# Kernel optimization log

Hardware: AMD Instinct MI355X
Metric: run time of the kernel (lower is better)

## Reference

```python
import jax, jax.numpy as jnp
import numpy as np

D_MODEL = 1024
N_HEADS = 16
D_HEAD = D_MODEL // N_HEADS


def setup_inputs() -> dict:
    key = jax.random.key(0)
    kx, kq, kk, kv = jax.random.split(key, 4)
    B, T = 2, 2048
    X = jax.random.normal(kx, (B, T, D_MODEL), dtype=jnp.float32)
    s = 1.0 / np.sqrt(D_MODEL)
    # torch nn.Linear weight is [out, in]; y = x @ W.T
    Wq = jax.random.uniform(kq, (D_MODEL, D_MODEL), jnp.float32, -s, s)
    Wk = jax.random.uniform(kk, (D_MODEL, D_MODEL), jnp.float32, -s, s)
    Wv = jax.random.uniform(kv, (D_MODEL, D_MODEL), jnp.float32, -s, s)
    return {"X": X, "Wq": Wq, "Wk": Wk, "Wv": Wv}


def reference(X, Wq, Wk, Wv):
    B, T, _ = X.shape
    def heads(W):
        # x @ W.T -> [B,T,D] -> [B,H,T,Dh]
        return (X @ W.T).reshape(B, T, N_HEADS, D_HEAD).transpose(0, 2, 1, 3)
    Q, K, V = heads(Wq), heads(Wk), heads(Wv)
    scores = jnp.einsum('bhqd,bhkd->bhqk', Q, K)
    causal = jnp.tril(jnp.ones((T, T), dtype=bool))
    # original masks with -inf BEFORE scaling; -inf/scale == -inf, so equivalent
    scores = jnp.where(causal, scores, -jnp.inf) / jnp.sqrt(jnp.float32(D_HEAD))
    attn = jax.nn.softmax(scores, axis=-1)
    out = jnp.einsum('bhqk,bhkd->bhqd', attn, V)
    return out.transpose(0, 2, 1, 3).reshape(B, T, N_HEADS * D_HEAD)
```

## Files before the change

### kernel.cpp

```cpp
#include <hip/hip_runtime.h>


using bf16x8   = __attribute__((ext_vector_type(8))) __bf16;
using floatx4  = __attribute__((ext_vector_type(4))) float;
using floatx16 = __attribute__((ext_vector_type(16))) float;
using uintx4   = __attribute__((ext_vector_type(4))) unsigned int;

#define T_SEQ   2048
#define D_MODEL 1024
#define N_HEADS 16
#define D_HEAD  64
#define BATCH   2
#define M_TOT   4096
#define N_TOT   3072
#define PLANE   (T_SEQ * D_HEAD)
#define NX      (M_TOT * D_MODEL)
#define NWSEG   (D_MODEL * D_MODEL)
#define QSCALE  0.18033688f
#define SM_BIAS 24.0f

__device__ __forceinline__ unsigned short f32_to_bf16(float f) {
  unsigned int u = __float_as_uint(f);
  u += 0x7fffu + ((u >> 16) & 1u);
  return (unsigned short)(u >> 16);
}
__device__ __forceinline__ unsigned int pack2_bf16(float a, float b) {
  unsigned int ua = __float_as_uint(a) + 0x8000u;
  unsigned int ub = __float_as_uint(b) + 0x8000u;
  return __builtin_amdgcn_perm(ub, ua, 0x07060302);
}
__device__ __forceinline__ void async_cp16(void* lds, const void* gptr) {
  __builtin_amdgcn_global_load_lds(
      (const __attribute__((address_space(1))) unsigned int*)gptr,
      (__attribute__((address_space(3))) unsigned int*)lds, 16, 0, 0);
}

__global__ __launch_bounds__(256) void cvt_kernel(
    const float* __restrict__ X,  const float* __restrict__ Wq,
    const float* __restrict__ Wk, const float* __restrict__ Wv,
    unsigned short* __restrict__ Xb, unsigned short* __restrict__ Wb)
{
  const size_t i = ((size_t)blockIdx.x * 256 + threadIdx.x) * 8;
  const float* src;
  unsigned short* dst;
  if (i < NX) { src = X + i; dst = Xb + i; }
  else {
    const size_t r = i - NX;
    const int w = (int)(r >> 20);
    const size_t o = r & (NWSEG - 1);
    src = ((w == 0) ? Wq : (w == 1) ? Wk : Wv) + o;
    dst = Wb + r;
  }
  float4 f0 = *(const float4*)src;
  float4 f1 = *(const float4*)(src + 4);
  uint4 out;
  out.x = pack2_bf16(f0.x, f0.y);
  out.y = pack2_bf16(f0.z, f0.w);
  out.z = pack2_bf16(f1.x, f1.y);
  out.w = pack2_bf16(f1.z, f1.w);
  *(uint4*)dst = out;
}

__global__ __launch_bounds__(256) void gemm_qkv(
    const unsigned short* __restrict__ Xb,
    const unsigned short* __restrict__ Wb,
    unsigned short* __restrict__ Qb,
    unsigned short* __restrict__ Kb,
    unsigned short* __restrict__ VTb)
{
  __shared__ unsigned short Als[128 * 64];
  __shared__ unsigned short Bls[128 * 64];

  const int tid  = threadIdx.x;
  const int lane = tid & 63;
  const int wave = tid >> 6;
  const int l15  = lane & 15;
  const int quad = lane >> 4;
  const int wm   = wave >> 1, wn = wave & 1;

  const int n_blk = blockIdx.x * 128;
  const int m_blk = blockIdx.y * 128;

  const int swz = (((tid >> 3) ^ tid) & 7) * 8;
  const unsigned short* Ag = Xb + (size_t)(m_blk + (tid >> 3)) * D_MODEL + swz;
  const unsigned short* Bg = Wb + (size_t)(n_blk + (tid >> 3)) * D_MODEL + swz;
  char* Alds = (char*)Als + wave * 1024;
  char* Blds = (char*)Bls + wave * 1024;

  floatx4 acc[4][4] = {};

  for (int k0 = 0; k0 < D_MODEL; k0 += 64) {
    __syncthreads();
#pragma unroll
    for (int p = 0; p < 4; p++) {
      async_cp16(Alds + p * 4096, Ag + (size_t)p * 32 * D_MODEL + k0);
      async_cp16(Blds + p * 4096, Bg + (size_t)p * 32 * D_MODEL + k0);
    }
    __syncthreads();

#pragma unroll
    for (int ks = 0; ks < 2; ks++) {
      bf16x8 a[4], b[4];
#pragma unroll
      for (int i = 0; i < 4; i++) {
        const int sa = ((ks * 4 + quad) ^ (l15 & 7)) * 16;
        a[i] = *(const bf16x8*)((char*)Als + (wm * 64 + 16 * i + l15) * 128 + sa);
        b[i] = *(const bf16x8*)((char*)Bls + (wn * 64 + 16 * i + l15) * 128 + sa);
      }
#pragma unroll
      for (int mi = 0; mi < 4; mi++)
#pragma unroll
        for (int ni = 0; ni < 4; ni++)
          acc[mi][ni] = __builtin_amdgcn_mfma_f32_16x16x32_bf16(a[mi], b[ni], acc[mi][ni], 0, 0, 0);
    }
  }

  __syncthreads();
  char* ep = (char*)Als + wave * 8192;
  const int w_sel  = n_blk >> 10;
  const int m_base = m_blk + wm * 64;
  const int n_base = n_blk + wn * 64;
  const int h      = (n_base & 1023) >> 6;
  const float csc  = (w_sel == 0) ? QSCALE : 1.0f;

  if (w_sel < 2) {
#pragma unroll
    for (int mi = 0; mi < 4; mi++)
#pragma unroll
      for (int ni = 0; ni < 4; ni++)
#pragma unroll
        for (int r = 0; r < 4; r++) {
          const int row  = 16 * mi + quad * 4 + r;
          const int colb = (16 * ni + l15) * 2;
          const int phys = ((colb >> 4) ^ (row & 7)) * 16;
          *(unsigned short*)(ep + row * 128 + phys + (colb & 15)) =
              f32_to_bf16(acc[mi][ni][r] * csc);
        }
  } else {
#pragma unroll
    for (int mi = 0; mi < 4; mi++)
#pragma unroll
      for (int ni = 0; ni < 4; ni++)
#pragma unroll
        for (int r = 0; r < 4; r++) {
          const int row  = 16 * ni + l15;
          const int colb = (16 * mi + quad * 4 + r) * 2;
          const int phys = ((colb >> 4) ^ (row & 7)) * 16;
          *(unsigned short*)(ep + row * 128 + phys + (colb & 15)) =
              f32_to_bf16(acc[mi][ni][r]);
        }
  }
  asm volatile("s_waitcnt lgkmcnt(0)" ::: "memory");

#pragma unroll
  for (int pass = 0; pass < 8; pass++) {
    const int row  = pass * 8 + (lane >> 3);
    const int phys = ((lane & 7) ^ (row & 7)) * 16;
    uint4 v = *(const uint4*)(ep + row * 128 + phys);
    if (w_sel < 2) {
      const int m  = m_base + row;
      const int bb = m >> 11;
      const int t  = m & (T_SEQ - 1);
      unsigned short* dst = ((w_sel == 0) ? Qb : Kb) +
          ((size_t)(bb * N_HEADS + h) * T_SEQ + t) * D_HEAD + (lane & 7) * 8;
      *(uint4*)dst = v;
    } else {
      const int bb = m_base >> 11;
      unsigned short* dst = VTb +
          ((size_t)(bb * N_HEADS + h) * D_HEAD + row) * T_SEQ + (m_base & (T_SEQ - 1)) + (lane & 7) * 8;
      *(uint4*)dst = v;
    }
  }
}

__global__ __launch_bounds__(256) void attn_kernel(
    const unsigned short* __restrict__ Qb,
    const unsigned short* __restrict__ Kb,
    const unsigned short* __restrict__ VTb,
    float* __restrict__ Out)
{
  __shared__ __align__(16) char smem[65536];

  const int tid  = threadIdx.x;
  const int lane = tid & 63;
  const int wave = tid >> 6;
  const int l31  = lane & 31;
  const int q1   = lane >> 5;
  const int wq   = wave & 1;
  const int wk   = wave >> 1;

  const int bh   = blockIdx.x & 31;
  const int pair = blockIdx.x >> 5;

  const unsigned short* Qp = Qb  + (size_t)bh * PLANE;
  const unsigned short* Kp = Kb  + (size_t)bh * PLANE;
  const unsigned short* Vp = VTb + (size_t)bh * PLANE;

  const int swz = (((tid >> 3) ^ tid) & 7) * 8;
  const unsigned short* Kg = Kp + (size_t)(tid >> 3) * D_HEAD + swz;
  const unsigned short* Vg = Vp + (size_t)(tid >> 3) * T_SEQ + swz;
  const int b = bh >> 4, h = bh & 15;

  float* const LB = (float*)(smem + 33792);

#define STAGE_CHUNK(c)                                                        \
  do {                                                                        \
    char* kd = smem + (((c) >> 1) & 1) * 16384 + ((c) & 1) * 8192;            \
    char* vd = smem + 32768 + (((c) >> 1) & 1) * 16384 + ((c) & 1) * 8192;    \
    _Pragma("unroll")                                                         \
    for (int p = 0; p < 2; p++) {                                             \
      async_cp16(kd + p * 4096 + wave * 1024,                                 \
                 Kg + (size_t)((c) * 64 + p * 32) * D_HEAD);                  \
      async_cp16(vd + p * 4096 + wave * 1024,                                 \
                 Vg + (size_t)(p * 32) * T_SEQ + (c) * 64);                   \
    }                                                                         \
  } while (0)

#pragma unroll 1
  for (int it = 0; it < 2; it++) {
    const int strip = it ? (31 - pair) : pair;
    const int qbase = strip * 64 + wq * 32;
    const int nch   = strip + 1;

    bf16x8 aq[4];
#pragma unroll
    for (int kp = 0; kp < 4; kp++)
      aq[kp] = *(const bf16x8*)(Qp + (size_t)(qbase + l31) * D_HEAD + kp * 16 + q1 * 8);

    floatx16 o0 = {}, o1 = {};
    float l_acc = 0.0f;

    __syncthreads();

    STAGE_CHUNK(0);
    if (nch > 1) STAGE_CHUNK(1);

#pragma unroll 1
    for (int j2 = 0; j2 < nch; j2 += 2) {
      __syncthreads();
      if (j2 + 2 < nch) STAGE_CHUNK(j2 + 2);
      if (j2 + 3 < nch) STAGE_CHUNK(j2 + 3);

#pragma unroll
      for (int u = 0; u < 2; u++) {
        const int jc = j2 + u;
        if (jc >= nch) break;
        const char* Ksb = smem + ((jc >> 1) & 1) * 16384 + (jc & 1) * 8192;
        const char* Vsb = smem + 32768 + ((jc >> 1) & 1) * 16384 + (jc & 1) * 8192;
        const int kbase = jc * 64 + wk * 32;

        if (kbase <= qbase + 31) {
          floatx16 s = {};
          const int krow = wk * 32 + l31;
          __builtin_amdgcn_s_setprio(1);
#pragma unroll
          for (int kp = 0; kp < 4; kp++) {
            const int phys = (((2 * kp + q1) ^ (krow & 7)) * 16);
            bf16x8 ak = *(const bf16x8*)(Ksb + krow * 128 + phys);
            s = __builtin_amdgcn_mfma_f32_32x32x16_bf16(ak, aq[kp], s, 0, 0, 0);
          }
          __builtin_amdgcn_s_setprio(0);

          if (kbase >= qbase) {
            const int q = qbase + l31;
#pragma unroll
            for (int r = 0; r < 16; r++) {
              const int kk = kbase + (r & 3) + 8 * (r >> 2) + 4 * q1;
              if (kk > q) s[r] = -INFINITY;
            }
          }

          float pv[16];
#pragma unroll
          for (int r = 0; r < 16; r++)
            pv[r] = __builtin_amdgcn_exp2f(s[r] - SM_BIAS);
#pragma unroll
          for (int r = 0; r < 16; r += 4)
            l_acc += (pv[r] + pv[r + 1]) + (pv[r + 2] + pv[r + 3]);

          unsigned int w[8];
#pragma unroll
          for (int m = 0; m < 8; m++)
            asm("v_cvt_pk_bf16_f32 %0, %1, %2" : "=v"(w[m]) : "v"(pv[2 * m]), "v"(pv[2 * m + 1]));

          __builtin_amdgcn_s_setprio(1);
#pragma unroll
          for (int kp = 0; kp < 2; kp++) {
            unsigned int b0 = w[4 * kp],     b2 = w[4 * kp + 2];
            unsigned int b1 = w[4 * kp + 1], b3 = w[4 * kp + 3];
            asm("v_permlane32_swap_b32 %0, %1" : "+v"(b0), "+v"(b2));
            asm("v_permlane32_swap_b32 %0, %1" : "+v"(b1), "+v"(b3));
            uintx4 uu; uu[0] = b0; uu[1] = b1; uu[2] = b2; uu[3] = b3;
            const bf16x8 pf = __builtin_bit_cast(bf16x8, uu);

            const int c = 4 * wk + 2 * kp + q1;
            const int row0 = l31;
            bf16x8 av0 = *(const bf16x8*)(Vsb + row0 * 128 + ((c ^ (row0 & 7)) * 16));
            o0 = __builtin_amdgcn_mfma_f32_32x32x16_bf16(av0, pf, o0, 0, 0, 0);
            const int row1 = 32 + l31;
            bf16x8 av1 = *(const bf16x8*)(Vsb + row1 * 128 + ((c ^ (row1 & 7)) * 16));
            o1 = __builtin_amdgcn_mfma_f32_32x32x16_bf16(av1, pf, o1, 0, 0, 0);
          }
          __builtin_amdgcn_s_setprio(0);
        }
      }
    }

    float la = l_acc, lb2 = l_acc;
    asm("v_permlane32_swap_b32 %0, %1" : "+v"(la), "+v"(lb2));
    const float lt = la + lb2;

    __syncthreads();

    float* ob = (float*)smem + (wk * 2 + wq) * (64 * 33);
#pragma unroll
    for (int r = 0; r < 16; r++) {
      const int d0 = (r & 3) + 8 * (r >> 2) + 4 * q1;
      ob[d0 * 33 + l31]        = o0[r];
      ob[(32 + d0) * 33 + l31] = o1[r];
    }
    if (lane < 32) LB[wk * 64 + wq * 32 + l31] = lt;
    __syncthreads();

    const int row = tid >> 2;
    const int dg  = tid & 3;
    const int wqr = row >> 5, ql = row & 31;
    const float inv = 1.0f / (LB[row] + LB[64 + row]);
    const float* obA = (const float*)smem + (0 * 2 + wqr) * (64 * 33);
    const float* obB = (const float*)smem + (1 * 2 + wqr) * (64 * 33);

    float vout[16];
#pragma unroll
    for (int i = 0; i < 16; i++) {
      const int d = dg * 16 + i;
      vout[i] = (obA[d * 33 + ql] + obB[d * 33 + ql]) * inv;
    }
    const int t = strip * 64 + row;
    float* dst = Out + (size_t)(b * T_SEQ + t) * D_MODEL + h * D_HEAD + dg * 16;
#pragma unroll
    for (int m = 0; m < 4; m++)
      *(float4*)(dst + 4 * m) = *(const float4*)(vout + 4 * m);
  }
#undef STAGE_CHUNK
}

extern "C" void kernel_launch(void* const* d_in, const int* in_sizes, int n_in,
                              void* d_out, int out_size, void* d_ws, size_t ws_size,
                              hipStream_t stream) {
  const float* X  = (const float*)d_in[0];
  const float* Wq = (const float*)d_in[1];
  const float* Wk = (const float*)d_in[2];
  const float* Wv = (const float*)d_in[3];

  unsigned short* Qb = (unsigned short*)d_ws;
  unsigned short* Kb = Qb + (size_t)BATCH * N_HEADS * T_SEQ * D_HEAD;
  unsigned short* VT = Kb + (size_t)BATCH * N_HEADS * T_SEQ * D_HEAD;

  unsigned short* Xb = (unsigned short*)d_out;
  unsigned short* Wb = Xb + (size_t)NX;

  cvt_kernel<<<3584, 256, 0, stream>>>(X, Wq, Wk, Wv, Xb, Wb);

  dim3 g1(N_TOT / 128, M_TOT / 128);
  gemm_qkv<<<g1, 256, 0, stream>>>(Xb, Wb, Qb, Kb, VT);

  attn_kernel<<<512, 256, 0, stream>>>(Qb, Kb, VT, (float*)d_out);
}
```

Baseline: 149.8 us.

## Split attention into 32-query strips with four waves splitting keys

The attention kernel now gives each block a 32-row query strip instead of 64 rows. All four waves share the same queries and each takes a different 32-key slice of a 128-key chunk, and the grid doubles to 1024 blocks. The multi-chunk async double-buffered K/V staging is replaced by a single 128-key buffer that is loaded and synchronized every iteration. This cuts LDS use and raises block count and occupancy, but it loses overlap between loads and compute, adds two barriers per chunk, and makes the final cross-wave reduction four-way.

```diff
diff --git a/kernel.cpp b/kernel.cpp
--- a/kernel.cpp
+++ b/kernel.cpp
@@ -179,15 +179,13 @@
     const unsigned short* __restrict__ VTb,
     float* __restrict__ Out)
 {
-  __shared__ __align__(16) char smem[65536];
+  __shared__ __align__(16) char smem[34304];
 
   const int tid  = threadIdx.x;
   const int lane = tid & 63;
   const int wave = tid >> 6;
   const int l31  = lane & 31;
   const int q1   = lane >> 5;
-  const int wq   = wave & 1;
-  const int wk   = wave >> 1;
 
   const int bh   = blockIdx.x & 31;
   const int pair = blockIdx.x >> 5;
@@ -195,32 +193,22 @@
   const unsigned short* Qp = Qb  + (size_t)bh * PLANE;
   const unsigned short* Kp = Kb  + (size_t)bh * PLANE;
   const unsigned short* Vp = VTb + (size_t)bh * PLANE;
-
-  const int swz = (((tid >> 3) ^ tid) & 7) * 8;
-  const unsigned short* Kg = Kp + (size_t)(tid >> 3) * D_HEAD + swz;
-  const unsigned short* Vg = Vp + (size_t)(tid >> 3) * T_SEQ + swz;
   const int b = bh >> 4, h = bh & 15;
 
+  const int sl4 = ((tid & 15) ^ (tid >> 4)) & 15;
+  const unsigned short* Kg0 =
+      Kp + (size_t)((tid >> 4) + 64 * (sl4 >> 3)) * D_HEAD + (sl4 & 7) * 8;
+  const unsigned short* Vg0 = Vp + (size_t)(tid >> 4) * T_SEQ + sl4 * 8;
+
+  char* const Ks = smem;
+  char* const Vs = smem + 16384;
   float* const LB = (float*)(smem + 33792);
-
-#define STAGE_CHUNK(c)                                                        \
-  do {                                                                        \
-    char* kd = smem + (((c) >> 1) & 1) * 16384 + ((c) & 1) * 8192;            \
-    char* vd = smem + 32768 + (((c) >> 1) & 1) * 16384 + ((c) & 1) * 8192;    \
-    _Pragma("unroll")                                                         \
-    for (int p = 0; p < 2; p++) {                                             \
-      async_cp16(kd + p * 4096 + wave * 1024,                                 \
-                 Kg + (size_t)((c) * 64 + p * 32) * D_HEAD);                  \
-      async_cp16(vd + p * 4096 + wave * 1024,                                 \
-                 Vg + (size_t)(p * 32) * T_SEQ + (c) * 64);                   \
-    }                                                                         \
-  } while (0)
 
 #pragma unroll 1
   for (int it = 0; it < 2; it++) {
-    const int strip = it ? (31 - pair) : pair;
-    const int qbase = strip * 64 + wq * 32;
-    const int nch   = strip + 1;
+    const int strip = it ? (63 - pair) : pair;
+    const int qbase = strip * 32;
+    const int nch   = (strip >> 2) + 1;
 
     bf16x8 aq[4];
 #pragma unroll
@@ -230,80 +218,75 @@
     floatx16 o0 = {}, o1 = {};
     float l_acc = 0.0f;
 
-    __syncthreads();
-
-    STAGE_CHUNK(0);
-    if (nch > 1) STAGE_CHUNK(1);
-
 #pragma unroll 1
-    for (int j2 = 0; j2 < nch; j2 += 2) {
+    for (int jc = 0; jc < nch; jc++) {
       __syncthreads();
-      if (j2 + 2 < nch) STAGE_CHUNK(j2 + 2);
-      if (j2 + 3 < nch) STAGE_CHUNK(j2 + 3);
-
-#pragma unroll
-      for (int u = 0; u < 2; u++) {
-        const int jc = j2 + u;
-        if (jc >= nch) break;
-        const char* Ksb = smem + ((jc >> 1) & 1) * 16384 + (jc & 1) * 8192;
-        const char* Vsb = smem + 32768 + ((jc >> 1) & 1) * 16384 + (jc & 1) * 8192;
-        const int kbase = jc * 64 + wk * 32;
-
-        if (kbase <= qbase + 31) {
-          floatx16 s = {};
-          const int krow = wk * 32 + l31;
-          __builtin_amdgcn_s_setprio(1);
-#pragma unroll
-          for (int kp = 0; kp < 4; kp++) {
-            const int phys = (((2 * kp + q1) ^ (krow & 7)) * 16);
-            bf16x8 ak = *(const bf16x8*)(Ksb + krow * 128 + phys);
-            s = __builtin_amdgcn_mfma_f32_32x32x16_bf16(ak, aq[kp], s, 0, 0, 0);
-          }
-          __builtin_amdgcn_s_setprio(0);
-
-          if (kbase >= qbase) {
-            const int q = qbase + l31;
-#pragma unroll
-            for (int r = 0; r < 16; r++) {
-              const int kk = kbase + (r & 3) + 8 * (r >> 2) + 4 * q1;
-              if (kk > q) s[r] = -INFINITY;
-            }
-          }
-
-          float pv[16];
-#pragma unroll
-          for (int r = 0; r < 16; r++)
-            pv[r] = __builtin_amdgcn_exp2f(s[r] - SM_BIAS);
-#pragma unroll
-          for (int r = 0; r < 16; r += 4)
-            l_acc += (pv[r] + pv[r + 1]) + (pv[r + 2] + pv[r + 3]);
-
-          unsigned int w[8];
-#pragma unroll
-          for (int m = 0; m < 8; m++)
-            asm("v_cvt_pk_bf16_f32 %0, %1, %2" : "=v"(w[m]) : "v"(pv[2 * m]), "v"(pv[2 * m + 1]));
-
-          __builtin_amdgcn_s_setprio(1);
-#pragma unroll
-          for (int kp = 0; kp < 2; kp++) {
-            unsigned int b0 = w[4 * kp],     b2 = w[4 * kp + 2];
-            unsigned int b1 = w[4 * kp + 1], b3 = w[4 * kp + 3];
-            asm("v_permlane32_swap_b32 %0, %1" : "+v"(b0), "+v"(b2));
-            asm("v_permlane32_swap_b32 %0, %1" : "+v"(b1), "+v"(b3));
-            uintx4 uu; uu[0] = b0; uu[1] = b1; uu[2] = b2; uu[3] = b3;
-            const bf16x8 pf = __builtin_bit_cast(bf16x8, uu);
-
-            const int c = 4 * wk + 2 * kp + q1;
-            const int row0 = l31;
-            bf16x8 av0 = *(const bf16x8*)(Vsb + row0 * 128 + ((c ^ (row0 & 7)) * 16));
-            o0 = __builtin_amdgcn_mfma_f32_32x32x16_bf16(av0, pf, o0, 0, 0, 0);
-            const int row1 = 32 + l31;
-            bf16x8 av1 = *(const bf16x8*)(Vsb + row1 * 128 + ((c ^ (row1 & 7)) * 16));
-            o1 = __builtin_amdgcn_mfma_f32_32x32x16_bf16(av1, pf, o1, 0, 0, 0);
-          }
-          __builtin_amdgcn_s_setprio(0);
+#pragma unroll
+      for (int p = 0; p < 4; p++) {
+        async_cp16(Ks + p * 4096 + wave * 1024,
+                   Kg0 + (size_t)jc * (128 * D_HEAD) + p * 16 * D_HEAD);
+        async_cp16(Vs + p * 4096 + wave * 1024,
+                   Vg0 + (size_t)p * 16 * T_SEQ + jc * 128);
+      }
+      __syncthreads();
+
+      const int kbase = jc * 128 + wave * 32;
+      if (kbase > qbase + 31) continue;
+
+      floatx16 s = {};
+      {
+        const int kloc = wave * 32 + l31;
+        const int line = kloc & 63;
+        const int chi  = (kloc >> 6) << 3;
+        __builtin_amdgcn_s_setprio(1);
+#pragma unroll
+        for (int kp = 0; kp < 4; kp++) {
+          const int c = chi | (kp * 2 + q1);
+          bf16x8 ak = *(const bf16x8*)(Ks + line * 256 + ((c ^ (line & 15)) * 16));
+          s = __builtin_amdgcn_mfma_f32_32x32x16_bf16(ak, aq[kp], s, 0, 0, 0);
         }
-      }
+        __builtin_amdgcn_s_setprio(0);
+      }
+
+      if (kbase >= qbase) {
+        const int q = qbase + l31;
+#pragma unroll
+        for (int r = 0; r < 16; r++) {
+          const int kk = kbase + (r & 3) + 8 * (r >> 2) + 4 * q1;
+          if (kk > q) s[r] = -INFINITY;
+        }
+      }
+
+      float pv[16];
+#pragma unroll
+      for (int r = 0; r < 16; r++)
+        pv[r] = __builtin_amdgcn_exp2f(s[r] - SM_BIAS);
+#pragma unroll
+      for (int r = 0; r < 16; r += 4)
+        l_acc += (pv[r] + pv[r + 1]) + (pv[r + 2] + pv[r + 3]);
+
+      unsigned int w[8];
+#pragma unroll
+      for (int m = 0; m < 8; m++)
+        asm("v_cvt_pk_bf16_f32 %0, %1, %2" : "=v"(w[m]) : "v"(pv[2 * m]), "v"(pv[2 * m + 1]));
+
+      __builtin_amdgcn_s_setprio(1);
+#pragma unroll
+      for (int kp = 0; kp < 2; kp++) {
+        unsigned int b0 = w[4 * kp],     b2 = w[4 * kp + 2];
+        unsigned int b1 = w[4 * kp + 1], b3 = w[4 * kp + 3];
+        asm("v_permlane32_swap_b32 %0, %1" : "+v"(b0), "+v"(b2));
+        asm("v_permlane32_swap_b32 %0, %1" : "+v"(b1), "+v"(b3));
+        uintx4 uu; uu[0] = b0; uu[1] = b1; uu[2] = b2; uu[3] = b3;
+        const bf16x8 pf = __builtin_bit_cast(bf16x8, uu);
+
+        const int cv = 4 * wave + 2 * kp + q1;
+        bf16x8 av0 = *(const bf16x8*)(Vs + l31 * 256 + ((cv ^ (l31 & 15)) * 16));
+        o0 = __builtin_amdgcn_mfma_f32_32x32x16_bf16(av0, pf, o0, 0, 0, 0);
+        bf16x8 av1 = *(const bf16x8*)(Vs + (32 + l31) * 256 + ((cv ^ (l31 & 15)) * 16));
+        o1 = __builtin_amdgcn_mfma_f32_32x32x16_bf16(av1, pf, o1, 0, 0, 0);
+      }
+      __builtin_amdgcn_s_setprio(0);
     }
 
     float la = l_acc, lb2 = l_acc;
@@ -312,36 +295,34 @@
 
     __syncthreads();
 
-    float* ob = (float*)smem + (wk * 2 + wq) * (64 * 33);
+    float* ob = (float*)smem + wave * (64 * 33);
 #pragma unroll
     for (int r = 0; r < 16; r++) {
       const int d0 = (r & 3) + 8 * (r >> 2) + 4 * q1;
       ob[d0 * 33 + l31]        = o0[r];
       ob[(32 + d0) * 33 + l31] = o1[r];
     }
-    if (lane < 32) LB[wk * 64 + wq * 32 + l31] = lt;
+    if (lane < 32) LB[wave * 32 + l31] = lt;
     __syncthreads();
 
-    const int row = tid >> 2;
-    const int dg  = tid & 3;
-    const int wqr = row >> 5, ql = row & 31;
-    const float inv = 1.0f / (LB[row] + LB[64 + row]);
-    const float* obA = (const float*)smem + (0 * 2 + wqr) * (64 * 33);
-    const float* obB = (const float*)smem + (1 * 2 + wqr) * (64 * 33);
-
-    float vout[16];
-#pragma unroll
-    for (int i = 0; i < 16; i++) {
-      const int d = dg * 16 + i;
-      vout[i] = (obA[d * 33 + ql] + obB[d * 33 + ql]) * inv;
-    }
-    const int t = strip * 64 + row;
-    float* dst = Out + (size_t)(b * T_SEQ + t) * D_MODEL + h * D_HEAD + dg * 16;
-#pragma unroll
-    for (int m = 0; m < 4; m++)
-      *(float4*)(dst + 4 * m) = *(const float4*)(vout + 4 * m);
-  }
-#undef STAGE_CHUNK
+    const int row = tid >> 3;
+    const int dg  = tid & 7;
+    const float inv = 1.0f / ((LB[row] + LB[32 + row]) + (LB[64 + row] + LB[96 + row]));
+    const float* o_base = (const float*)smem;
+
+    float vout[8];
+#pragma unroll
+    for (int i = 0; i < 8; i++) {
+      const int d = dg * 8 + i;
+      float acc = (o_base[0 * (64 * 33) + d * 33 + row] + o_base[1 * (64 * 33) + d * 33 + row]) +
+                  (o_base[2 * (64 * 33) + d * 33 + row] + o_base[3 * (64 * 33) + d * 33 + row]);
+      vout[i] = acc * inv;
+    }
+    const int t = strip * 32 + row;
+    float* dst = Out + (size_t)(b * T_SEQ + t) * D_MODEL + h * D_HEAD + dg * 8;
+    *(float4*)(dst)     = *(const float4*)(vout);
+    *(float4*)(dst + 4) = *(const float4*)(vout + 4);
+  }
 }
 
 extern "C" void kernel_launch(void* const* d_in, const int* in_sizes, int n_in,
@@ -364,5 +345,5 @@
   dim3 g1(N_TOT / 128, M_TOT / 128);
   gemm_qkv<<<g1, 256, 0, stream>>>(Xb, Wb, Qb, Kb, VT);
 
-  attn_kernel<<<512, 256, 0, stream>>>(Qb, Kb, VT, (float*)d_out);
-}
+  attn_kernel<<<1024, 256, 0, stream>>>(Qb, Kb, VT, (float*)d_out);
+}
```

Measured after the change: 158.9 us. 1.06x slower.
